# Kernel optimization log

Hardware: AMD Instinct MI355X
Metric: run time of the kernel (lower is better)

## Reference

```python
import jax, jax.numpy as jnp
import numpy as np

NEG = -1000.0   # mask value used by reduce_func for zero scores
SLOPE = 0.01    # default F.leaky_relu negative slope
N_NODES, N_EDGES, D_IN, D_OUT, N_HEADS = 100000, 1600000, 256, 64, 4


def setup_inputs() -> dict:
    key = jax.random.key(0)
    k0, k1, k2, k3, k4 = jax.random.split(key, 5)
    h = jax.random.normal(k0, (N_NODES, D_IN), jnp.float32)
    src = jax.random.randint(k1, (N_EDGES,), 0, N_NODES)
    dst = jax.random.randint(k2, (N_EDGES,), 0, N_NODES)
    # per-head fc weight [H, Din, Dout] and attn_fc weight [H, 2*Dout]
    W = jax.random.normal(k3, (N_HEADS, D_IN, D_OUT), jnp.float32) / np.sqrt(D_IN)
    att = jax.random.normal(k4, (N_HEADS, 2 * D_OUT), jnp.float32) / np.sqrt(2.0 * D_OUT)
    return {"h": h, "W": W, "att": att, "src": src, "dst": dst}


def reference(h, W, att, src, dst):
    N = h.shape[0]
    H, _, F = W.shape
    # per-head linear projection (dropout is identity in eval mode)
    z = jnp.einsum('nd,hdf->nhf', h, W)                      # [N,H,F]
    # leaky_relu([z_src||z_dst] @ a) == leaky_relu(z_src@a1 + z_dst@a2)
    a_src, a_dst = att[:, :F], att[:, F:]
    es = jnp.einsum('nhf,hf->nh', z, a_src)                  # [N,H]
    ed = jnp.einsum('nhf,hf->nh', z, a_dst)                  # [N,H]
    e = jax.nn.leaky_relu(es[src] + ed[dst], SLOPE)          # [E,H]
    # reduce_func replaces exact-zero scores with -1000 before softmax
    e = jnp.where(e == 0.0, NEG, e)
    # segment (per-destination) softmax, numerically stable
    m = jax.ops.segment_max(e, dst, num_segments=N)          # [N,H]
    m = jnp.where(jnp.isfinite(m), m, 0.0)                   # empty segments
    ex = jnp.exp(e - m[dst])                                 # [E,H]
    denom = jax.ops.segment_sum(ex, dst, num_segments=N)     # [N,H]
    safe = jnp.where(denom[dst] > 0.0, denom[dst], 1.0)
    alpha = ex / safe                                        # [E,H]
    # weighted scatter-sum of source features to destinations
    out = jax.ops.segment_sum(alpha[:, :, None] * z[src], dst, num_segments=N)  # [N,H,F]
    # merge='cat' over heads
    return out.reshape(N, H * F)
```

## Files before the change

kernel.cpp:

```cpp
#include <hip/hip_runtime.h>
#include <math.h>

#define NEGV (-1000.0f)
#define SLOPE 0.01f
#define D_IN 256
#define LDK 72

typedef _Float16 half8 __attribute__((ext_vector_type(8)));
typedef _Float16 half4h __attribute__((ext_vector_type(4)));
typedef float f32x4 __attribute__((ext_vector_type(4)));

__device__ __forceinline__ float rlf(float v, int l) {
    return __builtin_bit_cast(float, __builtin_amdgcn_readlane(__builtin_bit_cast(int, v), l));
}
__device__ __forceinline__ int rli(int v, int l) {
    return __builtin_amdgcn_readlane(v, l);
}

__global__ void wprep_kernel(const float* __restrict__ W, _Float16* __restrict__ Wt_hi,
                             _Float16* __restrict__ Wt_lo) {
    int i = blockIdx.x * 256 + threadIdx.x;
    int f = i & 63;
    int k = (i >> 6) & 255;
    int h = i >> 14;
    float w = W[i];
    _Float16 hi = (_Float16)w;
    _Float16 lo = (_Float16)(w - (float)hi);
    int c = f * 4 + h;
    Wt_hi[c * 256 + k] = hi;
    Wt_lo[c * 256 + k] = lo;
}

__global__ __launch_bounds__(512) void gemm_kernel(const float* __restrict__ hmat,
        const _Float16* __restrict__ Wt_hi, const _Float16* __restrict__ Wt_lo,
        float* __restrict__ z_t, int N) {
    __shared__ __align__(16) _Float16 smem[4 * 128 * LDK];
    _Float16* A_hi = smem;
    _Float16* A_lo = smem + 128 * LDK;
    _Float16* B_hi = smem + 2 * 128 * LDK;
    _Float16* B_lo = smem + 3 * 128 * LDK;
    const int t = threadIdx.x;
    const int lane = t & 63;
    const int w = t >> 6;
    const int quad = lane >> 4;
    const int m16 = lane & 15;
    const int rg = w & 3;
    const int cg = w >> 2;
    const int n0 = (blockIdx.x >> 1) * 128;
    const int c0 = (blockIdx.x & 1) * 128;

    f32x4 acc[2][4];
#pragma unroll
    for (int rt = 0; rt < 2; rt++)
#pragma unroll
        for (int ct = 0; ct < 4; ct++) acc[rt][ct] = (f32x4){0.f, 0.f, 0.f, 0.f};

    for (int kc = 0; kc < 256; kc += 64) {
        __syncthreads();
#pragma unroll
        for (int i = 0; i < 4; i++) {
            int idx = i * 512 + t;
            int row = idx >> 4, q = idx & 15;
            int rr = min(n0 + row, N - 1);
            float4 v = *(const float4*)&hmat[(size_t)rr * 256 + kc + q * 4];
            half4h hv, lv;
            hv[0] = (_Float16)v.x; lv[0] = (_Float16)(v.x - (float)hv[0]);
            hv[1] = (_Float16)v.y; lv[1] = (_Float16)(v.y - (float)hv[1]);
            hv[2] = (_Float16)v.z; lv[2] = (_Float16)(v.z - (float)hv[2]);
            hv[3] = (_Float16)v.w; lv[3] = (_Float16)(v.w - (float)hv[3]);
            *(half4h*)&A_hi[row * LDK + q * 4] = hv;
            *(half4h*)&A_lo[row * LDK + q * 4] = lv;
        }
#pragma unroll
        for (int i = 0; i < 2; i++) {
            int idx = i * 512 + t;
            int c = idx >> 3, seg = idx & 7;
            float4 vh = *(const float4*)&Wt_hi[(c0 + c) * 256 + kc + seg * 8];
            float4 vl = *(const float4*)&Wt_lo[(c0 + c) * 256 + kc + seg * 8];
            *(float4*)&B_hi[c * LDK + seg * 8] = vh;
            *(float4*)&B_lo[c * LDK + seg * 8] = vl;
        }
        __syncthreads();
#pragma unroll
        for (int ks = 0; ks < 2; ks++) {
            half8 ah[2], al[2], bh[4], bl[4];
#pragma unroll
            for (int rt = 0; rt < 2; rt++) {
                int ro = ((rg * 2 + rt) * 16 + m16) * LDK + ks * 32 + quad * 8;
                ah[rt] = *(const half8*)&A_hi[ro];
                al[rt] = *(const half8*)&A_lo[ro];
            }
#pragma unroll
            for (int ct = 0; ct < 4; ct++) {
                int co = ((cg * 4 + ct) * 16 + m16) * LDK + ks * 32 + quad * 8;
                bh[ct] = *(const half8*)&B_hi[co];
                bl[ct] = *(const half8*)&B_lo[co];
            }
#pragma unroll
            for (int rt = 0; rt < 2; rt++)
#pragma unroll
                for (int ct = 0; ct < 4; ct++) {
                    acc[rt][ct] = __builtin_amdgcn_mfma_f32_16x16x32_f16(ah[rt], bh[ct], acc[rt][ct], 0, 0, 0);
                    acc[rt][ct] = __builtin_amdgcn_mfma_f32_16x16x32_f16(al[rt], bh[ct], acc[rt][ct], 0, 0, 0);
                    acc[rt][ct] = __builtin_amdgcn_mfma_f32_16x16x32_f16(ah[rt], bl[ct], acc[rt][ct], 0, 0, 0);
                }
        }
    }
#pragma unroll
    for (int rt = 0; rt < 2; rt++)
#pragma unroll
        for (int ct = 0; ct < 4; ct++)
#pragma unroll
            for (int r = 0; r < 4; r++) {
                int n = n0 + rg * 32 + rt * 16 + quad * 4 + r;
                int c = c0 + cg * 64 + ct * 16 + m16;
                if (n < N) z_t[(size_t)n * 256 + c] = acc[rt][ct][r];
            }
}

__global__ void esed_kernel(float* __restrict__ z_t, const float* __restrict__ att,
                            float* __restrict__ es_ed, int N) {
    int gid = blockIdx.x * blockDim.x + threadIdx.x;
    int n = gid >> 6;
    int lane = gid & 63;
    if (n >= N) return;
    float4 zv = *(const float4*)&z_t[(size_t)n * 256 + lane * 4];
    float ps0 = zv.x * att[0 * 128 + lane];
    float ps1 = zv.y * att[1 * 128 + lane];
    float ps2 = zv.z * att[2 * 128 + lane];
    float ps3 = zv.w * att[3 * 128 + lane];
    float pd0 = zv.x * att[0 * 128 + 64 + lane];
    float pd1 = zv.y * att[1 * 128 + 64 + lane];
    float pd2 = zv.z * att[2 * 128 + 64 + lane];
    float pd3 = zv.w * att[3 * 128 + 64 + lane];
    for (int off = 1; off < 64; off <<= 1) {
        ps0 += __shfl_xor(ps0, off); ps1 += __shfl_xor(ps1, off);
        ps2 += __shfl_xor(ps2, off); ps3 += __shfl_xor(ps3, off);
        pd0 += __shfl_xor(pd0, off); pd1 += __shfl_xor(pd1, off);
        pd2 += __shfl_xor(pd2, off); pd3 += __shfl_xor(pd3, off);
    }
    half4h h16;
    h16[0] = (_Float16)zv.x; h16[1] = (_Float16)zv.y;
    h16[2] = (_Float16)zv.z; h16[3] = (_Float16)zv.w;
    *(half4h*)((_Float16*)z_t + (size_t)n * 512 + 256 + lane * 4) = h16;
    if (lane == 0) {
        *(float4*)&es_ed[(size_t)n * 8]     = make_float4(ps0, ps1, ps2, ps3);
        *(float4*)&es_ed[(size_t)n * 8 + 4] = make_float4(pd0, pd1, pd2, pd3);
    }
}

__global__ void hist_kernel(const int* __restrict__ dst, int* __restrict__ counts, int E) {
    int i = blockIdx.x * blockDim.x + threadIdx.x;
    if (i < E) atomicAdd(&counts[dst[i]], 1);
}

__global__ void scanA_kernel(const int* __restrict__ counts, int* __restrict__ bsums, int N) {
    __shared__ int lds[256];
    int t = threadIdx.x;
    int base = blockIdx.x * 1024 + t * 4;
    int s = 0;
    if (base + 3 < N) {
        int4 v = *(const int4*)&counts[base];
        s = v.x + v.y + v.z + v.w;
    } else {
        for (int u = 0; u < 4; u++) if (base + u < N) s += counts[base + u];
    }
    lds[t] = s; __syncthreads();
    for (int off = 128; off > 0; off >>= 1) {
        if (t < off) lds[t] += lds[t + off];
        __syncthreads();
    }
    if (t == 0) bsums[blockIdx.x] = lds[0];
}

__global__ void scanB_kernel(int* __restrict__ bsums, int nb) {
    __shared__ int lds[256];
    int t = threadIdx.x;
    int v = (t < nb) ? bsums[t] : 0;
    lds[t] = v; __syncthreads();
    for (int off = 1; off < 256; off <<= 1) {
        int x = (t >= off) ? lds[t - off] : 0;
        __syncthreads();
        lds[t] += x;
        __syncthreads();
    }
    if (t < nb) bsums[t] = lds[t] - v;
}

__global__ void scanC_kernel(const int* __restrict__ counts, const int* __restrict__ bsums,
                             int* __restrict__ row_start, int N) {
    __shared__ int lds[256];
    int t = threadIdx.x;
    int base = blockIdx.x * 1024 + t * 4;
    int4 v = make_int4(0, 0, 0, 0);
    if (base + 3 < N) v = *(const int4*)&counts[base];
    else {
        if (base + 0 < N) v.x = counts[base + 0];
        if (base + 1 < N) v.y = counts[base + 1];
        if (base + 2 < N) v.z = counts[base + 2];
    }
    int s = v.x + v.y + v.z + v.w;
    lds[t] = s; __syncthreads();
    for (int off = 1; off < 256; off <<= 1) {
        int x = (t >= off) ? lds[t - off] : 0;
        __syncthreads();
        lds[t] += x;
        __syncthreads();
    }
    int excl = lds[t] - s + bsums[blockIdx.x];
    int4 r;
    r.x = excl; r.y = r.x + v.x; r.z = r.y + v.y; r.w = r.z + v.z;
    if (base + 3 < N) *(int4*)&row_start[base] = r;
    else {
        if (base + 0 < N) row_start[base + 0] = r.x;
        if (base + 1 < N) row_start[base + 1] = r.y;
        if (base + 2 < N) row_start[base + 2] = r.z;
    }
}

__global__ void scatter_kernel(const int* __restrict__ src, const int* __restrict__ dst,
                               const int* __restrict__ row_start, int* __restrict__ cursor,
                               int* __restrict__ csr_src, int E) {
    int i = blockIdx.x * blockDim.x + threadIdx.x;
    if (i < E) {
        int d = dst[i];
        int pos = row_start[d] + atomicAdd(&cursor[d], 1);
        csr_src[pos] = src[i];
    }
}

__global__ __launch_bounds__(256) void aggregate_kernel(const _Float16* __restrict__ z16,
        const float* __restrict__ es_ed, const int* __restrict__ csr_src,
        const int* __restrict__ row_start, const int* __restrict__ counts,
        float* __restrict__ out, int N) {
    int gid = blockIdx.x * blockDim.x + threadIdx.x;
    int n = gid >> 6;
    int lane = gid & 63;
    if (n >= N) return;
    int cnt = counts[n];
    int start = row_start[n];
    float4 edn = *(const float4*)&es_ed[(size_t)n * 8 + 4];

    float m0 = -INFINITY, m1 = -INFINITY, m2 = -INFINITY, m3 = -INFINITY;
    float l0 = 0.f, l1 = 0.f, l2 = 0.f, l3 = 0.f;
    float4 o = make_float4(0.f, 0.f, 0.f, 0.f);

    for (int base = 0; base < cnt; base += 64) {
        int c = min(64, cnt - base);
        int i = base + lane;
        int s = 0;
        float e0 = -INFINITY, e1 = -INFINITY, e2 = -INFINITY, e3 = -INFINITY;
        if (i < cnt) {
            s = csr_src[start + i];
            float4 esv = *(const float4*)&es_ed[(size_t)s * 8];
            float x0 = esv.x + edn.x; e0 = x0 > 0.f ? x0 : SLOPE * x0; if (e0 == 0.f) e0 = NEGV;
            float x1 = esv.y + edn.y; e1 = x1 > 0.f ? x1 : SLOPE * x1; if (e1 == 0.f) e1 = NEGV;
            float x2 = esv.z + edn.z; e2 = x2 > 0.f ? x2 : SLOPE * x2; if (e2 == 0.f) e2 = NEGV;
            float x3 = esv.w + edn.w; e3 = x3 > 0.f ? x3 : SLOPE * x3; if (e3 == 0.f) e3 = NEGV;
        }
        float c0 = e0, c1 = e1, c2 = e2, c3 = e3;
        for (int off = 1; off < 64; off <<= 1) {
            c0 = fmaxf(c0, __shfl_xor(c0, off)); c1 = fmaxf(c1, __shfl_xor(c1, off));
            c2 = fmaxf(c2, __shfl_xor(c2, off)); c3 = fmaxf(c3, __shfl_xor(c3, off));
        }
        float nm0 = fmaxf(m0, c0), nm1 = fmaxf(m1, c1), nm2 = fmaxf(m2, c2), nm3 = fmaxf(m3, c3);
        float sc0 = __expf(m0 - nm0), sc1 = __expf(m1 - nm1);
        float sc2 = __expf(m2 - nm2), sc3 = __expf(m3 - nm3);
        o.x *= sc0; o.y *= sc1; o.z *= sc2; o.w *= sc3;
        l0 *= sc0; l1 *= sc1; l2 *= sc2; l3 *= sc3;
        m0 = nm0; m1 = nm1; m2 = nm2; m3 = nm3;

        float p0 = 0.f, p1 = 0.f, p2 = 0.f, p3 = 0.f;
        if (i < cnt) {
            p0 = __expf(e0 - m0); p1 = __expf(e1 - m1);
            p2 = __expf(e2 - m2); p3 = __expf(e3 - m3);
        }
        l0 += p0; l1 += p1; l2 += p2; l3 += p3;

        int j = 0;
        for (; j + 7 < c; j += 8) {
            float4 pp[8]; half4h zz[8];
#pragma unroll
            for (int u = 0; u < 8; u++) {
                int sj = rli(s, j + u);
                pp[u] = make_float4(rlf(p0, j + u), rlf(p1, j + u),
                                    rlf(p2, j + u), rlf(p3, j + u));
                zz[u] = *(const half4h*)&z16[(size_t)sj * 512 + 256 + lane * 4];
            }
#pragma unroll
            for (int u = 0; u < 8; u++) {
                o.x += pp[u].x * (float)zz[u][0]; o.y += pp[u].y * (float)zz[u][1];
                o.z += pp[u].z * (float)zz[u][2]; o.w += pp[u].w * (float)zz[u][3];
            }
        }
        for (; j < c; ++j) {
            int sj = rli(s, j);
            float q0 = rlf(p0, j), q1 = rlf(p1, j), q2 = rlf(p2, j), q3 = rlf(p3, j);
            half4h zv = *(const half4h*)&z16[(size_t)sj * 512 + 256 + lane * 4];
            o.x += q0 * (float)zv[0]; o.y += q1 * (float)zv[1];
            o.z += q2 * (float)zv[2]; o.w += q3 * (float)zv[3];
        }
    }
    for (int off = 1; off < 64; off <<= 1) {
        l0 += __shfl_xor(l0, off); l1 += __shfl_xor(l1, off);
        l2 += __shfl_xor(l2, off); l3 += __shfl_xor(l3, off);
    }
    if (cnt > 0) { o.x /= l0; o.y /= l1; o.z /= l2; o.w /= l3; }
    size_t ob = (size_t)n * 256;
    __builtin_nontemporal_store(o.x, &out[ob + lane]);
    __builtin_nontemporal_store(o.y, &out[ob + 64 + lane]);
    __builtin_nontemporal_store(o.z, &out[ob + 128 + lane]);
    __builtin_nontemporal_store(o.w, &out[ob + 192 + lane]);
}

extern "C" void kernel_launch(void* const* d_in, const int* in_sizes, int n_in,
                              void* d_out, int out_size, void* d_ws, size_t ws_size,
                              hipStream_t stream) {
    const float* hmat = (const float*)d_in[0];
    const float* W    = (const float*)d_in[1];
    const float* att  = (const float*)d_in[2];
    const int*   src  = (const int*)d_in[3];
    const int*   dst  = (const int*)d_in[4];
    int N = in_sizes[0] / D_IN;
    int E = in_sizes[3];
    float* out = (float*)d_out;

    float* z_t      = (float*)d_ws;
    float* es_ed    = z_t + (size_t)N * 256;
    _Float16* Wt_hi = (_Float16*)(es_ed + (size_t)N * 8);
    _Float16* Wt_lo = Wt_hi + 65536;
    int*   counts   = (int*)(Wt_lo + 65536);
    int*   cursor   = counts + N;
    int*   row_start= cursor + N;
    int*   bsums    = row_start + N;
    int*   csr_src  = bsums + 256;

    int NB = (N + 1023) / 1024;

    hipMemsetAsync(counts, 0, (size_t)2 * N * sizeof(int), stream);
    wprep_kernel<<<256, 256, 0, stream>>>(W, Wt_hi, Wt_lo);
    gemm_kernel<<<((N + 127) / 128) * 2, 512, 0, stream>>>(hmat, Wt_hi, Wt_lo, z_t, N);
    esed_kernel<<<(N * 64 + 255) / 256, 256, 0, stream>>>(z_t, att, es_ed, N);
    hist_kernel<<<(E + 255) / 256, 256, 0, stream>>>(dst, counts, E);
    scanA_kernel<<<NB, 256, 0, stream>>>(counts, bsums, N);
    scanB_kernel<<<1, 256, 0, stream>>>(bsums, NB);
    scanC_kernel<<<NB, 256, 0, stream>>>(counts, bsums, row_start, N);
    scatter_kernel<<<(E + 255) / 256, 256, 0, stream>>>(src, dst, row_start, cursor, csr_src, E);
    aggregate_kernel<<<(N * 64 + 255) / 256, 256, 0, stream>>>((const _Float16*)z_t, es_ed, csr_src, row_start, counts, out, N);
}
```

Before: 565.9 us.

## Pack two destination nodes per wave and precompute scatter slots in histogram

The aggregate kernel now handles two destination nodes per 64-lane wave, 32 lanes each. Each lane loads 8 fp16 features and writes paired nontemporal float2 stores. This targets idle lanes at low in-degree and fewer, wider gathers. The histogram kernel records each edge's atomic slot into unused workspace, so the scatter kernel needs no second atomic pass or cursor memset. The cost is extra slot traffic, and node pairs with unequal degrees cause divergence.

```diff
diff --git a/kernel.cpp b/kernel.cpp
--- a/kernel.cpp
+++ b/kernel.cpp
@@ -10,11 +10,12 @@
 typedef _Float16 half4h __attribute__((ext_vector_type(4)));
 typedef float f32x4 __attribute__((ext_vector_type(4)));
 
-__device__ __forceinline__ float rlf(float v, int l) {
-    return __builtin_bit_cast(float, __builtin_amdgcn_readlane(__builtin_bit_cast(int, v), l));
-}
 __device__ __forceinline__ int rli(int v, int l) {
     return __builtin_amdgcn_readlane(v, l);
+}
+__device__ __forceinline__ void nt_store2(float* p, float a, float b) {
+    float2 v = make_float2(a, b);
+    __builtin_nontemporal_store(__builtin_bit_cast(double, v), (double*)p);
 }
 
 __global__ void wprep_kernel(const float* __restrict__ W, _Float16* __restrict__ Wt_hi,
@@ -149,9 +150,13 @@
     }
 }
 
-__global__ void hist_kernel(const int* __restrict__ dst, int* __restrict__ counts, int E) {
+__global__ void hist_kernel(const int* __restrict__ dst, int* __restrict__ counts,
+                            int* __restrict__ slot, int E) {
     int i = blockIdx.x * blockDim.x + threadIdx.x;
-    if (i < E) atomicAdd(&counts[dst[i]], 1);
+    if (i < E) {
+        int sl = atomicAdd(&counts[dst[i]], 1);
+        slot[((i >> 7) << 8) + (i & 127)] = sl;
+    }
 }
 
 __global__ void scanA_kernel(const int* __restrict__ counts, int* __restrict__ bsums, int N) {
@@ -219,13 +224,12 @@
 }
 
 __global__ void scatter_kernel(const int* __restrict__ src, const int* __restrict__ dst,
-                               const int* __restrict__ row_start, int* __restrict__ cursor,
+                               const int* __restrict__ row_start, const int* __restrict__ slot,
                                int* __restrict__ csr_src, int E) {
     int i = blockIdx.x * blockDim.x + threadIdx.x;
     if (i < E) {
         int d = dst[i];
-        int pos = row_start[d] + atomicAdd(&cursor[d], 1);
-        csr_src[pos] = src[i];
+        csr_src[row_start[d] + slot[((i >> 7) << 8) + (i & 127)]] = src[i];
     }
 }
 
@@ -234,20 +238,26 @@
         const int* __restrict__ row_start, const int* __restrict__ counts,
         float* __restrict__ out, int N) {
     int gid = blockIdx.x * blockDim.x + threadIdx.x;
-    int n = gid >> 6;
+    int wv = gid >> 6;
     int lane = gid & 63;
-    if (n >= N) return;
-    int cnt = counts[n];
-    int start = row_start[n];
-    float4 edn = *(const float4*)&es_ed[(size_t)n * 8 + 4];
+    if (2 * wv >= N) return;
+    int half = lane >> 5;
+    int hl = lane & 31;
+    int n = 2 * wv + half;
+    int nn = min(n, N - 1);
+    int cnt = counts[nn];
+    int start = row_start[nn];
+    float4 edn = *(const float4*)&es_ed[(size_t)nn * 8 + 4];
+    int cmax = max(rli(cnt, 0), rli(cnt, 32));
+    int hb = half << 5;
 
     float m0 = -INFINITY, m1 = -INFINITY, m2 = -INFINITY, m3 = -INFINITY;
     float l0 = 0.f, l1 = 0.f, l2 = 0.f, l3 = 0.f;
-    float4 o = make_float4(0.f, 0.f, 0.f, 0.f);
-
-    for (int base = 0; base < cnt; base += 64) {
-        int c = min(64, cnt - base);
-        int i = base + lane;
+    float o0 = 0.f, o1 = 0.f, o2 = 0.f, o3 = 0.f;
+    float o4 = 0.f, o5 = 0.f, o6 = 0.f, o7 = 0.f;
+
+    for (int base = 0; base < cmax; base += 32) {
+        int i = base + hl;
         int s = 0;
         float e0 = -INFINITY, e1 = -INFINITY, e2 = -INFINITY, e3 = -INFINITY;
         if (i < cnt) {
@@ -259,14 +269,16 @@
             float x3 = esv.w + edn.w; e3 = x3 > 0.f ? x3 : SLOPE * x3; if (e3 == 0.f) e3 = NEGV;
         }
         float c0 = e0, c1 = e1, c2 = e2, c3 = e3;
-        for (int off = 1; off < 64; off <<= 1) {
+#pragma unroll
+        for (int off = 1; off < 32; off <<= 1) {
             c0 = fmaxf(c0, __shfl_xor(c0, off)); c1 = fmaxf(c1, __shfl_xor(c1, off));
             c2 = fmaxf(c2, __shfl_xor(c2, off)); c3 = fmaxf(c3, __shfl_xor(c3, off));
         }
         float nm0 = fmaxf(m0, c0), nm1 = fmaxf(m1, c1), nm2 = fmaxf(m2, c2), nm3 = fmaxf(m3, c3);
         float sc0 = __expf(m0 - nm0), sc1 = __expf(m1 - nm1);
         float sc2 = __expf(m2 - nm2), sc3 = __expf(m3 - nm3);
-        o.x *= sc0; o.y *= sc1; o.z *= sc2; o.w *= sc3;
+        o0 *= sc0; o1 *= sc1; o2 *= sc2; o3 *= sc3;
+        o4 *= sc0; o5 *= sc1; o6 *= sc2; o7 *= sc3;
         l0 *= sc0; l1 *= sc1; l2 *= sc2; l3 *= sc3;
         m0 = nm0; m1 = nm1; m2 = nm2; m3 = nm3;
 
@@ -277,40 +289,54 @@
         }
         l0 += p0; l1 += p1; l2 += p2; l3 += p3;
 
+        int jmax = min(32, cmax - base);
         int j = 0;
-        for (; j + 7 < c; j += 8) {
-            float4 pp[8]; half4h zz[8];
+        for (; j + 7 < jmax; j += 8) {
+            half8 zz[8]; float4 qq[8];
 #pragma unroll
             for (int u = 0; u < 8; u++) {
-                int sj = rli(s, j + u);
-                pp[u] = make_float4(rlf(p0, j + u), rlf(p1, j + u),
-                                    rlf(p2, j + u), rlf(p3, j + u));
-                zz[u] = *(const half4h*)&z16[(size_t)sj * 512 + 256 + lane * 4];
+                int idx = hb + j + u;
+                int ss = __shfl(s, idx);
+                qq[u] = make_float4(__shfl(p0, idx), __shfl(p1, idx),
+                                    __shfl(p2, idx), __shfl(p3, idx));
+                zz[u] = *(const half8*)&z16[(size_t)ss * 512 + 256 + hl * 8];
             }
 #pragma unroll
             for (int u = 0; u < 8; u++) {
-                o.x += pp[u].x * (float)zz[u][0]; o.y += pp[u].y * (float)zz[u][1];
-                o.z += pp[u].z * (float)zz[u][2]; o.w += pp[u].w * (float)zz[u][3];
-            }
-        }
-        for (; j < c; ++j) {
-            int sj = rli(s, j);
-            float q0 = rlf(p0, j), q1 = rlf(p1, j), q2 = rlf(p2, j), q3 = rlf(p3, j);
-            half4h zv = *(const half4h*)&z16[(size_t)sj * 512 + 256 + lane * 4];
-            o.x += q0 * (float)zv[0]; o.y += q1 * (float)zv[1];
-            o.z += q2 * (float)zv[2]; o.w += q3 * (float)zv[3];
-        }
-    }
-    for (int off = 1; off < 64; off <<= 1) {
+                o0 += qq[u].x * (float)zz[u][0]; o1 += qq[u].y * (float)zz[u][1];
+                o2 += qq[u].z * (float)zz[u][2]; o3 += qq[u].w * (float)zz[u][3];
+                o4 += qq[u].x * (float)zz[u][4]; o5 += qq[u].y * (float)zz[u][5];
+                o6 += qq[u].z * (float)zz[u][6]; o7 += qq[u].w * (float)zz[u][7];
+            }
+        }
+        for (; j < jmax; ++j) {
+            int idx = hb + j;
+            int ss = __shfl(s, idx);
+            float q0 = __shfl(p0, idx), q1 = __shfl(p1, idx);
+            float q2 = __shfl(p2, idx), q3 = __shfl(p3, idx);
+            half8 zv = *(const half8*)&z16[(size_t)ss * 512 + 256 + hl * 8];
+            o0 += q0 * (float)zv[0]; o1 += q1 * (float)zv[1];
+            o2 += q2 * (float)zv[2]; o3 += q3 * (float)zv[3];
+            o4 += q0 * (float)zv[4]; o5 += q1 * (float)zv[5];
+            o6 += q2 * (float)zv[6]; o7 += q3 * (float)zv[7];
+        }
+    }
+#pragma unroll
+    for (int off = 1; off < 32; off <<= 1) {
         l0 += __shfl_xor(l0, off); l1 += __shfl_xor(l1, off);
         l2 += __shfl_xor(l2, off); l3 += __shfl_xor(l3, off);
     }
-    if (cnt > 0) { o.x /= l0; o.y /= l1; o.z /= l2; o.w /= l3; }
-    size_t ob = (size_t)n * 256;
-    __builtin_nontemporal_store(o.x, &out[ob + lane]);
-    __builtin_nontemporal_store(o.y, &out[ob + 64 + lane]);
-    __builtin_nontemporal_store(o.z, &out[ob + 128 + lane]);
-    __builtin_nontemporal_store(o.w, &out[ob + 192 + lane]);
+    if (n < N) {
+        if (cnt > 0) {
+            o0 /= l0; o1 /= l1; o2 /= l2; o3 /= l3;
+            o4 /= l0; o5 /= l1; o6 /= l2; o7 /= l3;
+        }
+        float* ob = &out[(size_t)n * 256 + 2 * hl];
+        nt_store2(ob + 0,   o0, o4);
+        nt_store2(ob + 64,  o1, o5);
+        nt_store2(ob + 128, o2, o6);
+        nt_store2(ob + 192, o3, o7);
+    }
 }
 
 extern "C" void kernel_launch(void* const* d_in, const int* in_sizes, int n_in,
@@ -334,17 +360,19 @@
     int*   row_start= cursor + N;
     int*   bsums    = row_start + N;
     int*   csr_src  = bsums + 256;
+    int*   slot     = (int*)z_t;
 
     int NB = (N + 1023) / 1024;
-
-    hipMemsetAsync(counts, 0, (size_t)2 * N * sizeof(int), stream);
+    int aggBlocks = ((N + 1) / 2 + 3) / 4;
+
+    hipMemsetAsync(counts, 0, (size_t)N * sizeof(int), stream);
     wprep_kernel<<<256, 256, 0, stream>>>(W, Wt_hi, Wt_lo);
     gemm_kernel<<<((N + 127) / 128) * 2, 512, 0, stream>>>(hmat, Wt_hi, Wt_lo, z_t, N);
     esed_kernel<<<(N * 64 + 255) / 256, 256, 0, stream>>>(z_t, att, es_ed, N);
-    hist_kernel<<<(E + 255) / 256, 256, 0, stream>>>(dst, counts, E);
+    hist_kernel<<<(E + 255) / 256, 256, 0, stream>>>(dst, counts, slot, E);
     scanA_kernel<<<NB, 256, 0, stream>>>(counts, bsums, N);
     scanB_kernel<<<1, 256, 0, stream>>>(bsums, NB);
     scanC_kernel<<<NB, 256, 0, stream>>>(counts, bsums, row_start, N);
-    scatter_kernel<<<(E + 255) / 256, 256, 0, stream>>>(src, dst, row_start, cursor, csr_src, E);
-    aggregate_kernel<<<(N * 64 + 255) / 256, 256, 0, stream>>>((const _Float16*)z_t, es_ed, csr_src, row_start, counts, out, N);
-}
+    scatter_kernel<<<(E + 255) / 256, 256, 0, stream>>>(src, dst, row_start, slot, csr_src, E);
+    aggregate_kernel<<<aggBlocks, 256, 0, stream>>>((const _Float16*)z_t, es_ed, csr_src, row_start, counts, out, N);
+}
```

New measurement: 513.3 us. 1.1x faster.
